# Performance work log

Hardware: AMD Instinct MI355X
Metric: run time of the kernel (lower is better)

The kernel has to match this reference:

```python
import jax, jax.numpy as jnp
import numpy as np

D = 1024      # feature_dim / vertice_dim
H = 4         # n_heads
HD = D // H   # head dim 256
DFF = 2 * D   # 2048
DV = 1024     # vertice_dim
T = 64        # frame_num
PERIOD = 30
NEG = -1e9


def setup_inputs() -> dict:
    key = jax.random.key(0)
    ks = iter(jax.random.split(key, 32))
    sc = 0.02
    def w(shape):
        return jax.random.normal(next(ks), shape, dtype=jnp.float32) * sc
    return {
        "hidden_states": jax.random.normal(next(ks), (T, DV), dtype=jnp.float32),
        "hid_w": w((D, DV)), "hid_b": w((D,)),
        "obj_w": w((D, 80)),
        "sa_in_w": w((3 * D, D)), "sa_in_b": w((3 * D,)),
        "sa_out_w": w((D, D)), "sa_out_b": w((D,)),
        "ca_in_w": w((3 * D, D)), "ca_in_b": w((3 * D,)),
        "ca_out_w": w((D, D)), "ca_out_b": w((D,)),
        "ln1_g": jnp.ones((D,), jnp.float32), "ln1_b": jnp.zeros((D,), jnp.float32),
        "ln2_g": jnp.ones((D,), jnp.float32), "ln2_b": jnp.zeros((D,), jnp.float32),
        "ln3_g": jnp.ones((D,), jnp.float32), "ln3_b": jnp.zeros((D,), jnp.float32),
        "ff1_w": w((DFF, D)), "ff1_b": w((DFF,)),
        "ff2_w": w((D, DFF)), "ff2_b": w((D,)),
        "vr_w": w((DV, D)), "vr_b": w((DV,)),
        "vm_w": w((D, DV)), "vm_b": w((D,)),
    }


def _periodic_pe():
    # sin/cos PE over one period, tiled (PeriodicPositionalEncoding)
    pos = jnp.arange(PERIOD, dtype=jnp.float32)[:, None]
    div = jnp.exp(jnp.arange(0, D, 2, dtype=jnp.float32) * (-np.log(10000.0) / D))
    pe = jnp.zeros((PERIOD, D), jnp.float32)
    pe = pe.at[:, 0::2].set(jnp.sin(pos * div)).at[:, 1::2].set(jnp.cos(pos * div))
    reps = T // PERIOD + 1
    return jnp.tile(pe, (reps, 1))[:T]  # (T, D)


def reference(hidden_states, hid_w, hid_b, obj_w,
              sa_in_w, sa_in_b, sa_out_w, sa_out_b,
              ca_in_w, ca_in_b, ca_out_w, ca_out_b,
              ln1_g, ln1_b, ln2_g, ln2_b, ln3_g, ln3_b,
              ff1_w, ff1_b, ff2_w, ff2_b, vr_w, vr_b, vm_w, vm_b):
    mem = hidden_states @ hid_w.T + hid_b          # (S=T, D)
    style = obj_w[:, 0]                             # one-hot(0) @ obj_vector
    pe = _periodic_pe()

    # ALiBi-style biased causal mask (init_biased_mask, n_head=4)
    slopes = 0.25 ** jnp.arange(1, H + 1, dtype=jnp.float32)
    idx = jnp.arange(T)
    i_, j_ = idx[:, None], idx[None, :]
    alibi = -((i_ - j_) // PERIOD).astype(jnp.float32)
    tgt_bias = jnp.where(j_ <= i_, slopes[:, None, None] * alibi[None], NEG)  # (H,T,T)
    # vocaset enc_dec_mask: frame i may only attend memory frame i
    mem_bias = jnp.where(i_ == j_, 0.0, NEG)  # (T,S)

    def mha(q_in, kv_in, in_w, in_b, out_w, out_b, bias):
        wq, wk, wv = jnp.split(in_w, 3, axis=0)
        bq, bk, bv = jnp.split(in_b, 3)
        q = (q_in @ wq.T + bq).reshape(-1, H, HD)
        k = (kv_in @ wk.T + bk).reshape(-1, H, HD)
        v = (kv_in @ wv.T + bv).reshape(-1, H, HD)
        s = jnp.einsum('qhd,khd->hqk', q, k) / np.sqrt(HD) + bias
        a = jax.nn.softmax(s, axis=-1)
        o = jnp.einsum('hqk,khd->qhd', a, v).reshape(-1, D)
        return o @ out_w.T + out_b

    def ln(x, g, b):
        m = x.mean(-1, keepdims=True)
        v = ((x - m) ** 2).mean(-1, keepdims=True)
        return (x - m) / jnp.sqrt(v + 1e-5) * g + b

    def decode(x):  # post-norm TransformerDecoderLayer (eval, dropout off)
        x = ln(x + mha(x, x, sa_in_w, sa_in_b, sa_out_w, sa_out_b, tgt_bias), ln1_g, ln1_b)
        x = ln(x + mha(x, mem, ca_in_w, ca_in_b, ca_out_w, ca_out_b, mem_bias[None]), ln2_g, ln2_b)
        h = jax.nn.relu(x @ ff1_w.T + ff1_b) @ ff2_w.T + ff2_b
        return ln(x + h, ln3_g, ln3_b)

    # independent of the zero-padded future slots, matching the growing-seq loop.
    emb0 = jnp.zeros((T, D), jnp.float32).at[0].set(style)

    def step(emb, i):
        out = decode(emb + pe)
        new_tok = (out[i] @ vr_w.T + vr_b) @ vm_w.T + vm_b + style
        return emb.at[i + 1].set(new_tok), None

    emb, _ = jax.lax.scan(step, emb0, jnp.arange(T - 1))
    # final iteration's vertice_out over the full T-length sequence
    return decode(emb + pe) @ vr_w.T + vr_b  # (T, DV)
```

## Files before the change

### kernel.cpp

```cpp
#include <hip/hip_runtime.h>
#include <math.h>

#define DIM  1024
#define SEQ  64
#define HDIM 256
#define NBLK 256
#define SLOT_STRIDE 32

__device__ __forceinline__ float wsum(float v){
  v += __shfl_xor(v, 32, 64); v += __shfl_xor(v, 16, 64); v += __shfl_xor(v, 8, 64);
  v += __shfl_xor(v, 4, 64);  v += __shfl_xor(v, 2, 64);  v += __shfl_xor(v, 1, 64);
  return v;
}
__device__ __forceinline__ float wmax(float v){
  v = fmaxf(v, __shfl_xor(v, 32, 64)); v = fmaxf(v, __shfl_xor(v, 16, 64));
  v = fmaxf(v, __shfl_xor(v, 8, 64));  v = fmaxf(v, __shfl_xor(v, 4, 64));
  v = fmaxf(v, __shfl_xor(v, 2, 64));  v = fmaxf(v, __shfl_xor(v, 1, 64));
  return v;
}
__device__ __forceinline__ float2 breduce2(float va, float vb, float* red){
  int tid = threadIdx.x;
  va = wsum(va); vb = wsum(vb);
  if ((tid & 63) == 0){ red[(tid >> 6) * 2] = va; red[(tid >> 6) * 2 + 1] = vb; }
  __syncthreads();
  float ra = red[0] + red[2] + red[4] + red[6];
  float rb = red[1] + red[3] + red[5] + red[7];
  __syncthreads();
  return make_float2(ra, rb);
}

__device__ __forceinline__ float ldc(const float* p){
  return __hip_atomic_load(p, __ATOMIC_RELAXED, __HIP_MEMORY_SCOPE_AGENT);
}
__device__ __forceinline__ void stc(float* p, float v){
  __hip_atomic_store(p, v, __ATOMIC_RELAXED, __HIP_MEMORY_SCOPE_AGENT);
}
__device__ __forceinline__ void sta(unsigned* p, unsigned v){
  __hip_atomic_store(p, v, __ATOMIC_RELAXED, __HIP_MEMORY_SCOPE_AGENT);
}
__device__ __forceinline__ void spin_ge(unsigned* p, unsigned ep){
  unsigned spins = 0;
  while (__hip_atomic_load(p, __ATOMIC_RELAXED, __HIP_MEMORY_SCOPE_AGENT) < ep){
    __builtin_amdgcn_s_sleep(1);
    if (++spins > 100000000u) break;
  }
}

__device__ __forceinline__ void gsync(unsigned* bar, unsigned ep, int bid, int tid){
  unsigned* slots = bar;
  unsigned* gfl   = bar + 256 * SLOT_STRIDE;
  asm volatile("s_waitcnt vmcnt(0)" ::: "memory");
  __syncthreads();
  if (tid == 0) sta(&slots[bid * SLOT_STRIDE], ep);
  if (bid >= 240){
    int g = bid - 240;
    if (tid < 16) spin_ge(&slots[(g * 16 + tid) * SLOT_STRIDE], ep);
    __syncthreads();
    if (tid < 8) sta(&gfl[(g * 8 + tid) * SLOT_STRIDE], ep);
  }
  if (tid < 16) spin_ge(&gfl[(tid * 8 + (bid & 7)) * SLOT_STRIDE], ep);
  __syncthreads();
  asm volatile("" ::: "memory");
}

__global__ void mm1024(const float* __restrict__ A0, const float* __restrict__ B,
                       float* __restrict__ C0, size_t Astride, size_t Cstride){
  const float* A = A0 + (size_t)blockIdx.z * Astride;
  float* C = C0 + (size_t)blockIdx.z * Cstride;
  __shared__ float As[16][65];
  __shared__ float Bs[16][65];
  int ta = blockIdx.y * 64, tb = blockIdx.x * 64;
  int tx = threadIdx.x & 15, ty = threadIdx.x >> 4;
  float acc[4][4] = {};
  for (int k0 = 0; k0 < 1024; k0 += 16){
    #pragma unroll
    for (int j = 0; j < 4; ++j)
      As[tx][ty * 4 + j] = A[(size_t)(ta + ty * 4 + j) * 1024 + k0 + tx];
    {
      const float4 bv = *(const float4*)&B[(size_t)(k0 + ty) * 1024 + tb + tx * 4];
      Bs[ty][tx * 4]     = bv.x; Bs[ty][tx * 4 + 1] = bv.y;
      Bs[ty][tx * 4 + 2] = bv.z; Bs[ty][tx * 4 + 3] = bv.w;
    }
    __syncthreads();
    #pragma unroll
    for (int kk = 0; kk < 16; ++kk){
      float av[4], bv[4];
      #pragma unroll
      for (int m = 0; m < 4; ++m) av[m] = As[kk][ty * 4 + m];
      #pragma unroll
      for (int n = 0; n < 4; ++n) bv[n] = Bs[kk][tx * 4 + n];
      #pragma unroll
      for (int m = 0; m < 4; ++m)
        #pragma unroll
        for (int n = 0; n < 4; ++n) acc[m][n] = fmaf(av[m], bv[n], acc[m][n]);
    }
    __syncthreads();
  }
  #pragma unroll
  for (int m = 0; m < 4; ++m){
    float4 ov = { acc[m][0], acc[m][1], acc[m][2], acc[m][3] };
    *(float4*)&C[(size_t)(ta + ty * 4 + m) * 1024 + tb + tx * 4] = ov;
  }
}

struct CoopArgs {
  const float *hs, *hid_w, *hid_b;
  const float *sa_in_w, *sa_in_b, *sa_out_w, *sa_out_b;
  const float *ca_in_w, *ca_in_b, *ca_out_w, *ca_out_b;
  const float *ln1_g, *ln1_b, *ln2_g, *ln2_b, *ln3_g, *ln3_b;
  const float *ff1_w, *ff1_b, *ff2_w, *ff2_b;
  const float *vr_w, *vr_b, *vm_w, *vm_b, *obj_w;
  const float *Cm, *WqF, *WkF, *WvF;
  float *mem, *vtmp, *cac, *kc, *vcur, *q, *u, *hb, *w, *s;
  float *peT, *stylev, *cbvec, *wqpeT, *wkpeT, *wvpeT;
  float *out;
  unsigned *bar, *flags;
};

__global__ void __launch_bounds__(256, 2) decode_loop(CoopArgs a){
  const int tid = threadIdx.x, bid = blockIdx.x;
  const int wave = tid >> 6, lane = tid & 63;
  const int gw = bid * 4 + wave;
  __shared__ float smA[2048];
  __shared__ float smB[1024];
  __shared__ float smC[1024];
  __shared__ float scp[256];
  __shared__ float red[8];
  unsigned bep = 0;
  const float NLOG = -9.210340371976184f / 1024.0f;

  {
    float pw[16];
    const float* pr = a.hid_w + (size_t)gw * DIM;
    #pragma unroll
    for (int k = 0; k < 16; ++k) pw[k] = pr[lane + 64 * k];
    float bias = a.hid_b[gw];
    for (int t = 0; t < 64; ++t){
      const float* xr = a.hs + (size_t)t * DIM;
      float acc = 0.f;
      #pragma unroll
      for (int k = 0; k < 16; ++k) acc = fmaf(pw[k], xr[lane + 64 * k], acc);
      acc = wsum(acc);
      if (lane == 0) stc(a.mem + (size_t)t * DIM + gw, acc + bias);
    }
    if (bid < 30){
      int p = bid;
      for (int d = tid; d < DIM; d += 256){
        float dv = __expf((float)(2 * (d >> 1)) * NLOG);
        float arg = (float)p * dv;
        stc(a.peT + (size_t)p * DIM + d, (d & 1) ? cosf(arg) : sinf(arg));
      }
    } else if (bid == 30){
      for (int d = tid; d < DIM; d += 256) stc(a.stylev + d, a.obj_w[(size_t)d * 80]);
    }
  }
  ++bep; gsync(a.bar, bep, bid, tid);

  float cbv;
  {
    const float* pv = a.vm_w + (size_t)gw * DIM;
    float acc = 0.f;
    #pragma unroll
    for (int k = 0; k < 16; ++k) acc = fmaf(pv[lane + 64 * k], a.vr_b[lane + 64 * k], acc);
    acc = wsum(acc);
    cbv = acc + a.vm_b[gw] + ldc(a.stylev + gw);
    if (lane == 0) stc(a.cbvec + gw, cbv);
  }
  {
    float pw[16];
    const float* pr = a.ca_in_w + (size_t)(2 * DIM + gw) * DIM;
    #pragma unroll
    for (int k = 0; k < 16; ++k) pw[k] = pr[lane + 64 * k];
    float bias = a.ca_in_b[2 * DIM + gw];
    for (int t = 0; t < 64; ++t){
      const float* xr = a.mem + (size_t)t * DIM;
      #pragma unroll
      for (int k = 0; k < 4; ++k) smA[tid + 256 * k] = ldc(xr + tid + 256 * k);
      __syncthreads();
      float acc = 0.f;
      #pragma unroll
      for (int k = 0; k < 16; ++k) acc = fmaf(pw[k], smA[lane + 64 * k], acc);
      acc = wsum(acc);
      if (lane == 0) stc(a.vtmp + (size_t)t * DIM + gw, acc + bias);
      __syncthreads();
    }
  }
  ++bep; gsync(a.bar, bep, bid, tid);

  {
    float pw[16];
    const float* pr = a.ca_out_w + (size_t)gw * DIM;
    #pragma unroll
    for (int k = 0; k < 16; ++k) pw[k] = pr[lane + 64 * k];
    float bias = a.ca_out_b[gw];
    for (int t = 0; t < 64; ++t){
      const float* xr = a.vtmp + (size_t)t * DIM;
      #pragma unroll
      for (int k = 0; k < 4; ++k) smA[tid + 256 * k] = ldc(xr + tid + 256 * k);
      __syncthreads();
      float acc = 0.f;
      #pragma unroll
      for (int k = 0; k < 16; ++k) acc = fmaf(pw[k], smA[lane + 64 * k], acc);
      acc = wsum(acc);
      if (lane == 0) stc(a.cac + (size_t)t * DIM + gw, acc + bias);
      __syncthreads();
    }
  }
  ++bep; gsync(a.bar, bep, bid, tid);

  float aqcb, akcb, avcb, aq0, ak0, av0;
  {
    float wqr[16], wkr[16], wvr[16];
    const float* pq = a.sa_in_w + (size_t)gw * DIM;
    const float* pk = a.sa_in_w + (size_t)(DIM + gw) * DIM;
    const float* pv = a.sa_in_w + (size_t)(2 * DIM + gw) * DIM;
    #pragma unroll
    for (int k = 0; k < 16; ++k){
      int d = lane + 64 * k;
      wqr[k] = pq[d]; wkr[k] = pk[d]; wvr[k] = pv[d];
    }
    const float b_q = a.sa_in_b[gw];
    const float b_k = a.sa_in_b[DIM + gw];
    const float b_v = a.sa_in_b[2 * DIM + gw];
    #pragma unroll
    for (int k = 0; k < 4; ++k) smA[tid + 256 * k] = ldc(a.cbvec + tid + 256 * k);
    __syncthreads();
    float dq = 0.f, dk = 0.f, dv = 0.f;
    #pragma unroll
    for (int k = 0; k < 16; ++k){
      float x = smA[lane + 64 * k];
      dq = fmaf(wqr[k], x, dq); dk = fmaf(wkr[k], x, dk); dv = fmaf(wvr[k], x, dv);
    }
    aqcb = wsum(dq) + b_q; akcb = wsum(dk) + b_k; avcb = wsum(dv) + b_v;
    __syncthreads();
    #pragma unroll
    for (int k = 0; k < 4; ++k) smA[tid + 256 * k] = ldc(a.stylev + tid + 256 * k);
    __syncthreads();
    float sq = 0.f, sk = 0.f, sv = 0.f;
    #pragma unroll
    for (int k = 0; k < 16; ++k){
      float x = smA[lane + 64 * k];
      sq = fmaf(wqr[k], x, sq); sk = fmaf(wkr[k], x, sk); sv = fmaf(wvr[k], x, sv);
    }
    sq = wsum(sq); sk = wsum(sk); sv = wsum(sv);
    __syncthreads();
    float pq0 = 0.f, pk0 = 0.f, pv0 = 0.f;
    for (int p = 0; p < 30; ++p){
      #pragma unroll
      for (int k = 0; k < 4; ++k) smA[tid + 256 * k] = ldc(a.peT + (size_t)p * DIM + tid + 256 * k);
      __syncthreads();
      float tq = 0.f, tk = 0.f, tv = 0.f;
      #pragma unroll
      for (int k = 0; k < 16; ++k){
        float x = smA[lane + 64 * k];
        tq = fmaf(wqr[k], x, tq); tk = fmaf(wkr[k], x, tk); tv = fmaf(wvr[k], x, tv);
      }
      tq = wsum(tq); tk = wsum(tk); tv = wsum(tv);
      if (lane == 0){
        stc(a.wqpeT + (size_t)p * DIM + gw, tq);
        stc(a.wkpeT + (size_t)p * DIM + gw, tk);
        stc(a.wvpeT + (size_t)p * DIM + gw, tv);
      }
      if (p == 0){ pq0 = tq; pk0 = tk; pv0 = tv; }
      __syncthreads();
    }
    aq0 = sq + pq0 + b_q; ak0 = sk + pk0 + b_k; av0 = sv + pv0 + b_v;
  }
  ++bep; gsync(a.bar, bep, bid, tid);

  float fq[16], fk[16], fv[16], wo[16], f1a[16], f1b[16], f2[32];
  {
    const float* pq = a.WqF + (size_t)gw * DIM;
    const float* pk = a.WkF + (size_t)gw * DIM;
    const float* pv = a.WvF + (size_t)gw * DIM;
    const float* po = a.sa_out_w + (size_t)gw * DIM;
    const float* p1a = a.ff1_w + (size_t)(2 * gw) * DIM;
    const float* p1b = a.ff1_w + (size_t)(2 * gw + 1) * DIM;
    const float* p2 = a.ff2_w + (size_t)gw * 2048;
    #pragma unroll
    for (int k = 0; k < 16; ++k){
      int d = lane + 64 * k;
      fq[k] = pq[d]; fk[k] = pk[d]; fv[k] = pv[d]; wo[k] = po[d];
      f1a[k] = p1a[d]; f1b[k] = p1b[d];
    }
    #pragma unroll
    for (int k = 0; k < 32; ++k) f2[k] = p2[lane + 64 * k];
  }
  const float b_o  = a.sa_out_b[gw];
  const float b_1a = a.ff1_b[2 * gw];
  const float b_1b = a.ff1_b[2 * gw + 1];
  const float b_2  = a.ff2_b[gw];
  const float b_vr = a.vr_b[gw];

  float c0 = 0.f, c1 = 0.f, c2 = 0.f, c3 = 0.f;
  const bool is_score = (bid < 16);
  const int sc_h  = bid >> 2;
  const int sc_jg = bid & 3;
  const float sc_slope = 1.0f / (float)(4 << (2 * sc_h));

  float xres;
  if (lane == 0){
    stc(a.q + gw, aq0);
    stc(a.kc + gw, ak0);
    stc(a.vcur + gw, av0);
  }
  xres = a.obj_w[(size_t)gw * 80] + ldc(a.peT + gw);
  ++bep; gsync(a.bar, bep, bid, tid);

  float vrr[16], cmr[16];
  for (int i = 0; i < SEQ; ++i){
    const unsigned ep = (unsigned)(i + 1);

    {
      #pragma unroll
      for (int k = 0; k < 4; ++k){
        smB[tid + 256 * k] = ldc(a.vcur + tid + 256 * k);
        smC[tid + 256 * k] = ldc(a.q + tid + 256 * k);
      }
      __syncthreads();
      float p0 = 0.f, p1 = 0.f, p2 = 0.f, p3 = 0.f;
      #pragma unroll
      for (int k = 0; k < 4; ++k){
        p0 = fmaf(wo[k],      smB[lane + 64 * k],        p0);
        p1 = fmaf(wo[k + 4],  smB[lane + 64 * (k + 4)],  p1);
        p2 = fmaf(wo[k + 8],  smB[lane + 64 * (k + 8)],  p2);
        p3 = fmaf(wo[k + 12], smB[lane + 64 * (k + 12)], p3);
      }
      p0 = wsum(p0); p1 = wsum(p1); p2 = wsum(p2); p3 = wsum(p3);
      if (lane == i){ c0 = p0; c1 = p1; c2 = p2; c3 = p3; }
      if (is_score){
        #pragma unroll
        for (int jj = 0; jj < 4; ++jj){
          int j = sc_jg * 16 + wave * 4 + jj;
          if (j <= i){
            const float* kr = a.kc + (size_t)j * DIM + sc_h * HDIM;
            float acc = 0.f;
            #pragma unroll
            for (int m = 0; m < 4; ++m)
              acc = fmaf(smC[sc_h * HDIM + m * 64 + lane], ldc(kr + m * 64 + lane), acc);
            acc = wsum(acc);
            if (lane == 0)
              stc(a.s + sc_h * 64 + j, acc * 0.0625f - sc_slope * (float)((i - j) / 30));
          }
        }
        asm volatile("s_waitcnt vmcnt(0)" ::: "memory");
        __syncthreads();
        if (tid == 0){
          #pragma unroll
          for (int r = 0; r < 8; ++r)
            sta(&a.flags[(bid * 8 + r) * SLOT_STRIDE], ep);
        }
      }
      if (tid < 16) spin_ge(&a.flags[(tid * 8 + (bid & 7)) * SLOT_STRIDE], ep);
      __syncthreads();
      {
        const int h = wave;
        float sv = (lane <= i) ? ldc(a.s + h * 64 + lane) : -3.0e38f;
        float mx = wmax(sv);
        float p = (lane <= i) ? __expf(sv - mx) : 0.f;
        float sum = wsum(p);
        scp[h * 64 + lane] = p / sum;
      }
      __syncthreads();
      float t = scp[lane] * c0 + scp[64 + lane] * c1 + scp[128 + lane] * c2 + scp[192 + lane] * c3;
      t = wsum(t);
      if (lane == 0) stc(a.u + gw, xres + t + b_o);
      __syncthreads();
    }
    ++bep; gsync(a.bar, bep, bid, tid);

    float x2v;
    {
      float cr[4];
      #pragma unroll
      for (int k = 0; k < 4; ++k) cr[k] = ldc(a.cac + (size_t)i * DIM + tid + 256 * k);
      #pragma unroll
      for (int k = 0; k < 4; ++k) smA[tid + 256 * k] = ldc(a.u + tid + 256 * k);
      __syncthreads();
      float sa = 0.f, sb = 0.f;
      #pragma unroll
      for (int k = 0; k < 4; ++k){ float x = smA[tid + 256 * k]; sa += x; sb = fmaf(x, x, sb); }
      float2 r = breduce2(sa, sb, red);
      float mean = r.x * (1.f / 1024.f);
      float var  = r.y * (1.f / 1024.f) - mean * mean;
      float rs = 1.f / sqrtf(var + 1e-5f);
      float tv[4];
      float ta = 0.f, tb = 0.f;
      #pragma unroll
      for (int k = 0; k < 4; ++k){
        int d = tid + 256 * k;
        float x1 = (smA[d] - mean) * rs * a.ln1_g[d] + a.ln1_b[d];
        tv[k] = x1 + cr[k];
        ta += tv[k]; tb = fmaf(tv[k], tv[k], tb);
      }
      float2 r2v = breduce2(ta, tb, red);
      float mean2 = r2v.x * (1.f / 1024.f);
      float var2  = r2v.y * (1.f / 1024.f) - mean2 * mean2;
      float rs2 = 1.f / sqrtf(var2 + 1e-5f);
      #pragma unroll
      for (int k = 0; k < 4; ++k){
        int d = tid + 256 * k;
        smA[d] = (tv[k] - mean2) * rs2 * a.ln2_g[d] + a.ln2_b[d];
      }
      __syncthreads();
      x2v = smA[gw];
      float acc0 = 0.f, acc1 = 0.f;
      #pragma unroll
      for (int k = 0; k < 16; ++k){
        float x = smA[lane + 64 * k];
        acc0 = fmaf(f1a[k], x, acc0);
        acc1 = fmaf(f1b[k], x, acc1);
      }
      acc0 = wsum(acc0); acc1 = wsum(acc1);
      if (lane == 0){
        stc(a.hb + 2 * gw,     fmaxf(acc0 + b_1a, 0.f));
        stc(a.hb + 2 * gw + 1, fmaxf(acc1 + b_1b, 0.f));
      }
      __syncthreads();
    }
    ++bep; gsync(a.bar, bep, bid, tid);

    {
      const float* pr = a.vr_w + (size_t)gw * DIM;
      const float* pc = a.Cm + (size_t)gw * DIM;
      #pragma unroll
      for (int k = 0; k < 16; ++k){ vrr[k] = pr[lane + 64 * k]; cmr[k] = pc[lane + 64 * k]; }
      #pragma unroll
      for (int k = 0; k < 8; ++k) smA[tid + 256 * k] = ldc(a.hb + tid + 256 * k);
      __syncthreads();
      float acc = 0.f;
      #pragma unroll
      for (int k = 0; k < 32; ++k) acc = fmaf(f2[k], smA[lane + 64 * k], acc);
      acc = wsum(acc);
      if (lane == 0) stc(a.w + gw, x2v + acc + b_2);
      __syncthreads();
    }
    ++bep; gsync(a.bar, bep, bid, tid);

    {
      #pragma unroll
      for (int k = 0; k < 4; ++k) smA[tid + 256 * k] = ldc(a.w + tid + 256 * k);
      __syncthreads();
      float sa = 0.f, sb = 0.f;
      #pragma unroll
      for (int k = 0; k < 4; ++k){ float x = smA[tid + 256 * k]; sa += x; sb = fmaf(x, x, sb); }
      float2 r = breduce2(sa, sb, red);
      float mean = r.x * (1.f / 1024.f);
      float var  = r.y * (1.f / 1024.f) - mean * mean;
      float rs = 1.f / sqrtf(var + 1e-5f);
      float ov[4];
      #pragma unroll
      for (int k = 0; k < 4; ++k){
        int d = tid + 256 * k;
        ov[k] = (smA[d] - mean) * rs * a.ln3_g[d] + a.ln3_b[d];
      }
      __syncthreads();
      #pragma unroll
      for (int k = 0; k < 4; ++k) smA[tid + 256 * k] = ov[k];
      __syncthreads();
      float ar = 0.f, ac = 0.f, aqn = 0.f, akn = 0.f, avn = 0.f;
      #pragma unroll
      for (int k = 0; k < 16; ++k){
        float x = smA[lane + 64 * k];
        ar  = fmaf(vrr[k], x, ar);
        ac  = fmaf(cmr[k], x, ac);
        aqn = fmaf(fq[k], x, aqn);
        akn = fmaf(fk[k], x, akn);
        avn = fmaf(fv[k], x, avn);
      }
      ar = wsum(ar); ac = wsum(ac);
      aqn = wsum(aqn); akn = wsum(akn); avn = wsum(avn);
      if (lane == 0) a.out[(size_t)i * DIM + gw] = ar + b_vr;
      if (i < SEQ - 1){
        int pn = (i + 1) % 30;
        if (lane == 0){
          float tq = ldc(a.wqpeT + (size_t)pn * DIM + gw);
          float tk = ldc(a.wkpeT + (size_t)pn * DIM + gw);
          float tv = ldc(a.wvpeT + (size_t)pn * DIM + gw);
          stc(a.q + gw, aqn + aqcb + tq);
          stc(a.kc + (size_t)(i + 1) * DIM + gw, akn + akcb + tk);
          stc(a.vcur + gw, avn + avcb + tv);
        }
        xres = ac + cbv + ldc(a.peT + (size_t)pn * DIM + gw);
        __syncthreads();
        ++bep; gsync(a.bar, bep, bid, tid);
      }
    }
  }
}

extern "C" void kernel_launch(void* const* d_in, const int* in_sizes, int n_in,
                              void* d_out, int out_size, void* d_ws, size_t ws_size,
                              hipStream_t stream){
  const float* hs       = (const float*)d_in[0];
  const float* hid_w    = (const float*)d_in[1];
  const float* hid_b    = (const float*)d_in[2];
  const float* obj_w    = (const float*)d_in[3];
  const float* sa_in_w  = (const float*)d_in[4];
  const float* sa_in_b  = (const float*)d_in[5];
  const float* sa_out_w = (const float*)d_in[6];
  const float* sa_out_b = (const float*)d_in[7];
  const float* ca_in_w  = (const float*)d_in[8];
  const float* ca_in_b  = (const float*)d_in[9];
  const float* ca_out_w = (const float*)d_in[10];
  const float* ca_out_b = (const float*)d_in[11];
  const float* ln1_g    = (const float*)d_in[12];
  const float* ln1_b    = (const float*)d_in[13];
  const float* ln2_g    = (const float*)d_in[14];
  const float* ln2_b    = (const float*)d_in[15];
  const float* ln3_g    = (const float*)d_in[16];
  const float* ln3_b    = (const float*)d_in[17];
  const float* ff1_w    = (const float*)d_in[18];
  const float* ff1_b    = (const float*)d_in[19];
  const float* ff2_w    = (const float*)d_in[20];
  const float* ff2_b    = (const float*)d_in[21];
  const float* vr_w     = (const float*)d_in[22];
  const float* vr_b     = (const float*)d_in[23];
  const float* vm_w     = (const float*)d_in[24];
  const float* vm_b     = (const float*)d_in[25];

  float* ws = (float*)d_ws;
  float* mem    = ws;
  float* vtmp   = ws + 65536;
  float* cac    = ws + 131072;
  float* kc     = ws + 196608;
  float* vcur   = ws + 262144;
  float* q      = ws + 263168;
  float* u      = ws + 264192;
  float* hb     = ws + 265216;
  float* wv     = ws + 267264;
  float* sbuf   = ws + 268288;
  float* peT    = ws + 269312;
  float* stylev = ws + 300032;
  float* cbvec  = ws + 301056;
  float* wqpeT  = ws + 302080;
  float* wkpeT  = ws + 332800;
  float* wvpeT  = ws + 363520;
  unsigned* bar   = (unsigned*)(ws + 394240);
  unsigned* flags = bar + 384 * SLOT_STRIDE;
  float* Cm     = ws + 425984;
  float* WqF    = ws + 1474560;
  float* WkF    = ws + 2523136;
  float* WvF    = ws + 3571712;

  hipMemsetAsync((void*)bar, 0, 512 * SLOT_STRIDE * 4, stream);

  mm1024<<<dim3(16, 16, 1), 256, 0, stream>>>(vm_w, vr_w, Cm, 0, 0);
  mm1024<<<dim3(16, 16, 3), 256, 0, stream>>>(sa_in_w, Cm, WqF,
                                              (size_t)1024 * 1024, (size_t)1024 * 1024);

  CoopArgs A;
  A.hs = hs; A.hid_w = hid_w; A.hid_b = hid_b;
  A.sa_in_w = sa_in_w; A.sa_in_b = sa_in_b; A.sa_out_w = sa_out_w; A.sa_out_b = sa_out_b;
  A.ca_in_w = ca_in_w; A.ca_in_b = ca_in_b; A.ca_out_w = ca_out_w; A.ca_out_b = ca_out_b;
  A.ln1_g = ln1_g; A.ln1_b = ln1_b; A.ln2_g = ln2_g; A.ln2_b = ln2_b; A.ln3_g = ln3_g; A.ln3_b = ln3_b;
  A.ff1_w = ff1_w; A.ff1_b = ff1_b; A.ff2_w = ff2_w; A.ff2_b = ff2_b;
  A.vr_w = vr_w; A.vr_b = vr_b; A.vm_w = vm_w; A.vm_b = vm_b; A.obj_w = obj_w;
  A.Cm = Cm; A.WqF = WqF; A.WkF = WkF; A.WvF = WvF;
  A.mem = mem; A.vtmp = vtmp; A.cac = cac; A.kc = kc; A.vcur = vcur;
  A.q = q; A.u = u; A.hb = hb; A.w = wv; A.s = sbuf;
  A.peT = peT; A.stylev = stylev; A.cbvec = cbvec;
  A.wqpeT = wqpeT; A.wkpeT = wkpeT; A.wvpeT = wvpeT;
  A.out = (float*)d_out;
  A.bar = bar; A.flags = flags;

  void* params[1] = { &A };
  hipError_t e = hipLaunchCooperativeKernel((void*)decode_loop, dim3(NBLK), dim3(256), params, 0, stream);
  if (e != hipSuccess){
    decode_loop<<<dim3(NBLK), dim3(256), 0, stream>>>(A);
  }
}
```

Before: 2.267 ms.

## Replace grid barriers in decode loop with per-step sentinel dataflow polling

Removes the per-stage grid-wide barriers inside the 64-step autoregressive loop. Each intermediate buffer becomes per-step (indexed by i) and is pre-filled with a NaN sentinel, and consumers spin on the data itself until the sentinel is overwritten. The remaining barrier is simplified to a flat all-slot spin with no sleep, and the preamble vector reads go straight from global memory. This cuts barrier latency, but it relies on relaxed atomics for ordering, adds a sentinel-init kernel and larger workspace buffers, and produces heavy polling traffic.

Measured after the change: 2.049 ms. -9.6%, faster.

```diff
diff --git a/kernel.cpp b/kernel.cpp
--- a/kernel.cpp
+++ b/kernel.cpp
@@ -6,6 +6,7 @@
 #define HDIM 256
 #define NBLK 256
 #define SLOT_STRIDE 32
+#define SENTU 0xFFC00ABCu
 
 __device__ __forceinline__ float wsum(float v){
   v += __shfl_xor(v, 32, 64); v += __shfl_xor(v, 16, 64); v += __shfl_xor(v, 8, 64);
@@ -35,30 +36,35 @@
 __device__ __forceinline__ void stc(float* p, float v){
   __hip_atomic_store(p, v, __ATOMIC_RELAXED, __HIP_MEMORY_SCOPE_AGENT);
 }
-__device__ __forceinline__ void sta(unsigned* p, unsigned v){
-  __hip_atomic_store(p, v, __ATOMIC_RELAXED, __HIP_MEMORY_SCOPE_AGENT);
-}
+__device__ __forceinline__ float plc(const float* p){
+  float v = ldc(p);
+  unsigned s = 0;
+  while (__float_as_uint(v) == SENTU){ v = ldc(p); if (++s > 200000000u) break; }
+  return v;
+}
+__device__ __forceinline__ void poll4s(const float* p, int stride, float* out){
+  float v0 = ldc(p), v1 = ldc(p + stride), v2 = ldc(p + 2 * stride), v3 = ldc(p + 3 * stride);
+  unsigned s = 0;
+  while (__float_as_uint(v0) == SENTU || __float_as_uint(v1) == SENTU ||
+         __float_as_uint(v2) == SENTU || __float_as_uint(v3) == SENTU){
+    v0 = ldc(p); v1 = ldc(p + stride); v2 = ldc(p + 2 * stride); v3 = ldc(p + 3 * stride);
+    if (++s > 200000000u) break;
+  }
+  out[0] = v0; out[1] = v1; out[2] = v2; out[3] = v3;
+}
+
 __device__ __forceinline__ void spin_ge(unsigned* p, unsigned ep){
   unsigned spins = 0;
   while (__hip_atomic_load(p, __ATOMIC_RELAXED, __HIP_MEMORY_SCOPE_AGENT) < ep){
-    __builtin_amdgcn_s_sleep(1);
     if (++spins > 100000000u) break;
   }
 }
-
-__device__ __forceinline__ void gsync(unsigned* bar, unsigned ep, int bid, int tid){
-  unsigned* slots = bar;
-  unsigned* gfl   = bar + 256 * SLOT_STRIDE;
+__device__ __forceinline__ void gsync(unsigned* slots, unsigned ep, int bid, int tid){
   asm volatile("s_waitcnt vmcnt(0)" ::: "memory");
   __syncthreads();
-  if (tid == 0) sta(&slots[bid * SLOT_STRIDE], ep);
-  if (bid >= 240){
-    int g = bid - 240;
-    if (tid < 16) spin_ge(&slots[(g * 16 + tid) * SLOT_STRIDE], ep);
-    __syncthreads();
-    if (tid < 8) sta(&gfl[(g * 8 + tid) * SLOT_STRIDE], ep);
-  }
-  if (tid < 16) spin_ge(&gfl[(tid * 8 + (bid & 7)) * SLOT_STRIDE], ep);
+  if (tid == 0)
+    __hip_atomic_store(&slots[bid * SLOT_STRIDE], ep, __ATOMIC_RELAXED, __HIP_MEMORY_SCOPE_AGENT);
+  spin_ge(&slots[tid * SLOT_STRIDE], ep);
   __syncthreads();
   asm volatile("" ::: "memory");
 }
@@ -103,6 +109,11 @@
   }
 }
 
+__global__ void sentinit(unsigned* p, size_t n){
+  size_t idx = (size_t)blockIdx.x * 256 + threadIdx.x;
+  for (size_t k = idx; k < n; k += (size_t)gridDim.x * 256) p[k] = SENTU;
+}
+
 struct CoopArgs {
   const float *hs, *hid_w, *hid_b;
   const float *sa_in_w, *sa_in_b, *sa_out_w, *sa_out_b;
@@ -111,10 +122,11 @@
   const float *ff1_w, *ff1_b, *ff2_w, *ff2_b;
   const float *vr_w, *vr_b, *vm_w, *vm_b, *obj_w;
   const float *Cm, *WqF, *WkF, *WvF;
-  float *mem, *vtmp, *cac, *kc, *vcur, *q, *u, *hb, *w, *s;
+  float *mem, *vtmp, *cac;
+  float *kc, *qv, *vcB, *uB, *hbB, *wB, *sB;
   float *peT, *stylev, *cbvec, *wqpeT, *wkpeT, *wvpeT;
   float *out;
-  unsigned *bar, *flags;
+  unsigned *bar;
 };
 
 __global__ void __launch_bounds__(256, 2) decode_loop(CoopArgs a){
@@ -123,7 +135,6 @@
   const int gw = bid * 4 + wave;
   __shared__ float smA[2048];
   __shared__ float smB[1024];
-  __shared__ float smC[1024];
   __shared__ float scp[256];
   __shared__ float red[8];
   unsigned bep = 0;
@@ -208,7 +219,7 @@
   }
   ++bep; gsync(a.bar, bep, bid, tid);
 
-  float aqcb, akcb, avcb, aq0, ak0, av0;
+  float aqcb, akcb, avcb;
   {
     float wqr[16], wkr[16], wvr[16];
     const float* pq = a.sa_in_w + (size_t)gw * DIM;
@@ -222,37 +233,23 @@
     const float b_q = a.sa_in_b[gw];
     const float b_k = a.sa_in_b[DIM + gw];
     const float b_v = a.sa_in_b[2 * DIM + gw];
-    #pragma unroll
-    for (int k = 0; k < 4; ++k) smA[tid + 256 * k] = ldc(a.cbvec + tid + 256 * k);
-    __syncthreads();
-    float dq = 0.f, dk = 0.f, dv = 0.f;
+    float dq = 0.f, dk = 0.f, dv = 0.f, sq = 0.f, sk = 0.f, sv = 0.f;
     #pragma unroll
     for (int k = 0; k < 16; ++k){
-      float x = smA[lane + 64 * k];
-      dq = fmaf(wqr[k], x, dq); dk = fmaf(wkr[k], x, dk); dv = fmaf(wvr[k], x, dv);
+      float xc = ldc(a.cbvec + lane + 64 * k);
+      float xs = ldc(a.stylev + lane + 64 * k);
+      dq = fmaf(wqr[k], xc, dq); dk = fmaf(wkr[k], xc, dk); dv = fmaf(wvr[k], xc, dv);
+      sq = fmaf(wqr[k], xs, sq); sk = fmaf(wkr[k], xs, sk); sv = fmaf(wvr[k], xs, sv);
     }
     aqcb = wsum(dq) + b_q; akcb = wsum(dk) + b_k; avcb = wsum(dv) + b_v;
-    __syncthreads();
-    #pragma unroll
-    for (int k = 0; k < 4; ++k) smA[tid + 256 * k] = ldc(a.stylev + tid + 256 * k);
-    __syncthreads();
-    float sq = 0.f, sk = 0.f, sv = 0.f;
-    #pragma unroll
-    for (int k = 0; k < 16; ++k){
-      float x = smA[lane + 64 * k];
-      sq = fmaf(wqr[k], x, sq); sk = fmaf(wkr[k], x, sk); sv = fmaf(wvr[k], x, sv);
-    }
     sq = wsum(sq); sk = wsum(sk); sv = wsum(sv);
-    __syncthreads();
     float pq0 = 0.f, pk0 = 0.f, pv0 = 0.f;
     for (int p = 0; p < 30; ++p){
-      #pragma unroll
-      for (int k = 0; k < 4; ++k) smA[tid + 256 * k] = ldc(a.peT + (size_t)p * DIM + tid + 256 * k);
-      __syncthreads();
+      const float* pp = a.peT + (size_t)p * DIM;
       float tq = 0.f, tk = 0.f, tv = 0.f;
       #pragma unroll
       for (int k = 0; k < 16; ++k){
-        float x = smA[lane + 64 * k];
+        float x = ldc(pp + lane + 64 * k);
         tq = fmaf(wqr[k], x, tq); tk = fmaf(wkr[k], x, tk); tv = fmaf(wvr[k], x, tv);
       }
       tq = wsum(tq); tk = wsum(tk); tv = wsum(tv);
@@ -262,9 +259,12 @@
         stc(a.wvpeT + (size_t)p * DIM + gw, tv);
       }
       if (p == 0){ pq0 = tq; pk0 = tk; pv0 = tv; }
-      __syncthreads();
-    }
-    aq0 = sq + pq0 + b_q; ak0 = sk + pk0 + b_k; av0 = sv + pv0 + b_v;
+    }
+    if (lane == 0){
+      stc(a.qv + gw, sq + pq0 + b_q);
+      stc(a.kc + gw, sk + pk0 + b_k);
+      stc(a.vcB + gw, sv + pv0 + b_v);
+    }
   }
   ++bep; gsync(a.bar, bep, bid, tid);
 
@@ -298,25 +298,14 @@
   const int sc_jg = bid & 3;
   const float sc_slope = 1.0f / (float)(4 << (2 * sc_h));
 
-  float xres;
-  if (lane == 0){
-    stc(a.q + gw, aq0);
-    stc(a.kc + gw, ak0);
-    stc(a.vcur + gw, av0);
-  }
-  xres = a.obj_w[(size_t)gw * 80] + ldc(a.peT + gw);
-  ++bep; gsync(a.bar, bep, bid, tid);
-
+  float xres = a.obj_w[(size_t)gw * 80] + ldc(a.peT + gw);
   float vrr[16], cmr[16];
+
   for (int i = 0; i < SEQ; ++i){
-    const unsigned ep = (unsigned)(i + 1);
-
     {
-      #pragma unroll
-      for (int k = 0; k < 4; ++k){
-        smB[tid + 256 * k] = ldc(a.vcur + tid + 256 * k);
-        smC[tid + 256 * k] = ldc(a.q + tid + 256 * k);
-      }
+      float vv[4];
+      poll4s(a.vcB + (size_t)i * DIM + tid, 256, vv);
+      smB[tid] = vv[0]; smB[tid + 256] = vv[1]; smB[tid + 512] = vv[2]; smB[tid + 768] = vv[3];
       __syncthreads();
       float p0 = 0.f, p1 = 0.f, p2 = 0.f, p3 = 0.f;
       #pragma unroll
@@ -329,53 +318,43 @@
       p0 = wsum(p0); p1 = wsum(p1); p2 = wsum(p2); p3 = wsum(p3);
       if (lane == i){ c0 = p0; c1 = p1; c2 = p2; c3 = p3; }
       if (is_score){
+        float q4[4];
+        poll4s(a.qv + (size_t)i * DIM + sc_h * HDIM + lane, 64, q4);
         #pragma unroll
         for (int jj = 0; jj < 4; ++jj){
           int j = sc_jg * 16 + wave * 4 + jj;
           if (j <= i){
-            const float* kr = a.kc + (size_t)j * DIM + sc_h * HDIM;
+            const float* kr = a.kc + (size_t)j * DIM + sc_h * HDIM + lane;
             float acc = 0.f;
             #pragma unroll
-            for (int m = 0; m < 4; ++m)
-              acc = fmaf(smC[sc_h * HDIM + m * 64 + lane], ldc(kr + m * 64 + lane), acc);
+            for (int m = 0; m < 4; ++m) acc = fmaf(q4[m], plc(kr + m * 64), acc);
             acc = wsum(acc);
             if (lane == 0)
-              stc(a.s + sc_h * 64 + j, acc * 0.0625f - sc_slope * (float)((i - j) / 30));
+              stc(a.sB + (size_t)i * 256 + sc_h * 64 + j,
+                  acc * 0.0625f - sc_slope * (float)((i - j) / 30));
           }
         }
-        asm volatile("s_waitcnt vmcnt(0)" ::: "memory");
-        __syncthreads();
-        if (tid == 0){
-          #pragma unroll
-          for (int r = 0; r < 8; ++r)
-            sta(&a.flags[(bid * 8 + r) * SLOT_STRIDE], ep);
-        }
-      }
-      if (tid < 16) spin_ge(&a.flags[(tid * 8 + (bid & 7)) * SLOT_STRIDE], ep);
-      __syncthreads();
-      {
-        const int h = wave;
-        float sv = (lane <= i) ? ldc(a.s + h * 64 + lane) : -3.0e38f;
-        float mx = wmax(sv);
-        float p = (lane <= i) ? __expf(sv - mx) : 0.f;
-        float sum = wsum(p);
-        scp[h * 64 + lane] = p / sum;
-      }
+      }
+      float sv = (lane <= i) ? plc(a.sB + (size_t)i * 256 + wave * 64 + lane) : -3.0e38f;
+      float mx = wmax(sv);
+      float p = (lane <= i) ? __expf(sv - mx) : 0.f;
+      float sum = wsum(p);
+      scp[wave * 64 + lane] = p / sum;
       __syncthreads();
       float t = scp[lane] * c0 + scp[64 + lane] * c1 + scp[128 + lane] * c2 + scp[192 + lane] * c3;
       t = wsum(t);
-      if (lane == 0) stc(a.u + gw, xres + t + b_o);
-      __syncthreads();
-    }
-    ++bep; gsync(a.bar, bep, bid, tid);
+      if (lane == 0) stc(a.uB + (size_t)i * DIM + gw, xres + t + b_o);
+      __syncthreads();
+    }
 
     float x2v;
     {
       float cr[4];
       #pragma unroll
       for (int k = 0; k < 4; ++k) cr[k] = ldc(a.cac + (size_t)i * DIM + tid + 256 * k);
-      #pragma unroll
-      for (int k = 0; k < 4; ++k) smA[tid + 256 * k] = ldc(a.u + tid + 256 * k);
+      float uv[4];
+      poll4s(a.uB + (size_t)i * DIM + tid, 256, uv);
+      smA[tid] = uv[0]; smA[tid + 256] = uv[1]; smA[tid + 512] = uv[2]; smA[tid + 768] = uv[3];
       __syncthreads();
       float sa = 0.f, sb = 0.f;
       #pragma unroll
@@ -413,33 +392,35 @@
       }
       acc0 = wsum(acc0); acc1 = wsum(acc1);
       if (lane == 0){
-        stc(a.hb + 2 * gw,     fmaxf(acc0 + b_1a, 0.f));
-        stc(a.hb + 2 * gw + 1, fmaxf(acc1 + b_1b, 0.f));
-      }
-      __syncthreads();
-    }
-    ++bep; gsync(a.bar, bep, bid, tid);
+        stc(a.hbB + (size_t)i * 2048 + 2 * gw,     fmaxf(acc0 + b_1a, 0.f));
+        stc(a.hbB + (size_t)i * 2048 + 2 * gw + 1, fmaxf(acc1 + b_1b, 0.f));
+      }
+      __syncthreads();
+    }
 
     {
       const float* pr = a.vr_w + (size_t)gw * DIM;
       const float* pc = a.Cm + (size_t)gw * DIM;
       #pragma unroll
       for (int k = 0; k < 16; ++k){ vrr[k] = pr[lane + 64 * k]; cmr[k] = pc[lane + 64 * k]; }
-      #pragma unroll
-      for (int k = 0; k < 8; ++k) smA[tid + 256 * k] = ldc(a.hb + tid + 256 * k);
+      float h0[4], h1[4];
+      poll4s(a.hbB + (size_t)i * 2048 + tid, 256, h0);
+      poll4s(a.hbB + (size_t)i * 2048 + 1024 + tid, 256, h1);
+      #pragma unroll
+      for (int k = 0; k < 4; ++k){ smA[tid + 256 * k] = h0[k]; smA[tid + 1024 + 256 * k] = h1[k]; }
       __syncthreads();
       float acc = 0.f;
       #pragma unroll
       for (int k = 0; k < 32; ++k) acc = fmaf(f2[k], smA[lane + 64 * k], acc);
       acc = wsum(acc);
-      if (lane == 0) stc(a.w + gw, x2v + acc + b_2);
-      __syncthreads();
-    }
-    ++bep; gsync(a.bar, bep, bid, tid);
+      if (lane == 0) stc(a.wB + (size_t)i * DIM + gw, x2v + acc + b_2);
+      __syncthreads();
+    }
 
     {
-      #pragma unroll
-      for (int k = 0; k < 4; ++k) smA[tid + 256 * k] = ldc(a.w + tid + 256 * k);
+      float wv4[4];
+      poll4s(a.wB + (size_t)i * DIM + tid, 256, wv4);
+      smA[tid] = wv4[0]; smA[tid + 256] = wv4[1]; smA[tid + 512] = wv4[2]; smA[tid + 768] = wv4[3];
       __syncthreads();
       float sa = 0.f, sb = 0.f;
       #pragma unroll
@@ -477,14 +458,13 @@
           float tq = ldc(a.wqpeT + (size_t)pn * DIM + gw);
           float tk = ldc(a.wkpeT + (size_t)pn * DIM + gw);
           float tv = ldc(a.wvpeT + (size_t)pn * DIM + gw);
-          stc(a.q + gw, aqn + aqcb + tq);
+          stc(a.qv + (size_t)(i + 1) * DIM + gw, aqn + aqcb + tq);
           stc(a.kc + (size_t)(i + 1) * DIM + gw, akn + akcb + tk);
-          stc(a.vcur + gw, avn + avcb + tv);
+          stc(a.vcB + (size_t)(i + 1) * DIM + gw, avn + avcb + tv);
         }
         xres = ac + cbv + ldc(a.peT + (size_t)pn * DIM + gw);
-        __syncthreads();
-        ++bep; gsync(a.bar, bep, bid, tid);
-      }
+      }
+      __syncthreads();
     }
   }
 }
@@ -524,26 +504,26 @@
   float* vtmp   = ws + 65536;
   float* cac    = ws + 131072;
   float* kc     = ws + 196608;
-  float* vcur   = ws + 262144;
-  float* q      = ws + 263168;
-  float* u      = ws + 264192;
-  float* hb     = ws + 265216;
-  float* wv     = ws + 267264;
-  float* sbuf   = ws + 268288;
-  float* peT    = ws + 269312;
-  float* stylev = ws + 300032;
-  float* cbvec  = ws + 301056;
-  float* wqpeT  = ws + 302080;
-  float* wkpeT  = ws + 332800;
-  float* wvpeT  = ws + 363520;
-  unsigned* bar   = (unsigned*)(ws + 394240);
-  unsigned* flags = bar + 384 * SLOT_STRIDE;
-  float* Cm     = ws + 425984;
-  float* WqF    = ws + 1474560;
-  float* WkF    = ws + 2523136;
-  float* WvF    = ws + 3571712;
-
-  hipMemsetAsync((void*)bar, 0, 512 * SLOT_STRIDE * 4, stream);
+  float* qv     = ws + 262144;
+  float* vcB    = ws + 327680;
+  float* uB     = ws + 393216;
+  float* hbB    = ws + 458752;
+  float* wB     = ws + 589824;
+  float* sB     = ws + 655360;
+  float* peT    = ws + 671744;
+  float* stylev = ws + 702464;
+  float* cbvec  = ws + 703488;
+  float* wqpeT  = ws + 704512;
+  float* wkpeT  = ws + 735232;
+  float* wvpeT  = ws + 765952;
+  unsigned* bar = (unsigned*)(ws + 796672);
+  float* Cm     = ws + 804864;
+  float* WqF    = ws + 1853440;
+  float* WkF    = ws + 2902016;
+  float* WvF    = ws + 3950592;
+
+  hipMemsetAsync((void*)bar, 0, 256 * SLOT_STRIDE * 4, stream);
+  sentinit<<<512, 256, 0, stream>>>((unsigned*)kc, 475136);
 
   mm1024<<<dim3(16, 16, 1), 256, 0, stream>>>(vm_w, vr_w, Cm, 0, 0);
   mm1024<<<dim3(16, 16, 3), 256, 0, stream>>>(sa_in_w, Cm, WqF,
@@ -557,12 +537,12 @@
   A.ff1_w = ff1_w; A.ff1_b = ff1_b; A.ff2_w = ff2_w; A.ff2_b = ff2_b;
   A.vr_w = vr_w; A.vr_b = vr_b; A.vm_w = vm_w; A.vm_b = vm_b; A.obj_w = obj_w;
   A.Cm = Cm; A.WqF = WqF; A.WkF = WkF; A.WvF = WvF;
-  A.mem = mem; A.vtmp = vtmp; A.cac = cac; A.kc = kc; A.vcur = vcur;
-  A.q = q; A.u = u; A.hb = hb; A.w = wv; A.s = sbuf;
+  A.mem = mem; A.vtmp = vtmp; A.cac = cac;
+  A.kc = kc; A.qv = qv; A.vcB = vcB; A.uB = uB; A.hbB = hbB; A.wB = wB; A.sB = sB;
   A.peT = peT; A.stylev = stylev; A.cbvec = cbvec;
   A.wqpeT = wqpeT; A.wkpeT = wkpeT; A.wvpeT = wvpeT;
   A.out = (float*)d_out;
-  A.bar = bar; A.flags = flags;
+  A.bar = bar;
 
   void* params[1] = { &A };
   hipError_t e = hipLaunchCooperativeKernel((void*)decode_loop, dim3(NBLK), dim3(256), params, 0, stream);
```
